# Performance work log

Measured on AMD Instinct MI355X. Metric: run time of the kernel, lower is better.

Reference implementation:

```python
import jax, jax.numpy as jnp
import numpy as np
from jax import lax

SFREQ = 250.0
ORDER = 4
BANDS = [(4.0, 8.0), (8.0, 12.0), (12.0, 16.0), (16.0, 20.0), (20.0, 24.0), (24.0, 28.0), (28.0, 32.0), (32.0, 36.0), (36.0, 40.0)]
KLEN = int(SFREQ // 2)
if KLEN % 2 == 0:
    KLEN += 1  # 125 taps, odd -> same-length output with pad K//2


def _butter_bandpass(order, low, high, sfreq):
    # numpy reimplementation of scipy.signal.butter(order, [low,high]/nyq, btype='band')
    nyq = sfreq / 2.0
    fs = 2.0
    warped = 2.0 * fs * np.tan(np.pi * np.array([low, high]) / nyq / fs)
    m = np.arange(-order + 1, order, 2)
    p = -np.exp(1j * np.pi * m / (2 * order))  # analog Butterworth LP prototype poles
    k = 1.0
    bw = warped[1] - warped[0]
    wo = np.sqrt(warped[0] * warped[1])
    p_lp = p * bw / 2.0
    p_bp = np.concatenate([p_lp + np.sqrt(p_lp ** 2 - wo ** 2), p_lp - np.sqrt(p_lp ** 2 - wo ** 2)])
    z_bp = np.zeros(order, dtype=complex)
    k_bp = k * bw ** order
    fs2 = 2.0 * fs  # bilinear transform
    z_d = (fs2 + z_bp) / (fs2 - z_bp)
    p_d = (fs2 + p_bp) / (fs2 - p_bp)
    z_d = np.append(z_d, -np.ones(len(p_bp) - len(z_bp)))
    k_d = k_bp * np.real(np.prod(fs2 - z_bp) / np.prod(fs2 - p_bp))
    b = np.real(k_d * np.poly(z_d))
    a = np.real(np.poly(p_d))
    return b, a


def _make_kernel(low, high):
    # IIR impulse response (centered impulse, as in the torch module), Hann window, L1 normalize
    b, a = _butter_bandpass(ORDER, low, high, SFREQ)
    x = np.zeros(KLEN)
    x[KLEN // 2] = 1.0
    h = np.zeros(KLEN)
    for n in range(KLEN):
        s = 0.0
        for i in range(len(b)):
            if n - i >= 0:
                s += b[i] * x[n - i]
        for j in range(1, len(a)):
            if n - j >= 0:
                s -= a[j] * h[n - j]
        h[n] = s / a[0]
    nn = np.arange(KLEN)
    h = h * (0.5 - 0.5 * np.cos(2.0 * np.pi * nn / (KLEN - 1)))  # symmetric Hann
    return h / np.sum(np.abs(h))


def setup_inputs() -> dict:
    key = jax.random.key(0)
    x = jax.random.normal(key, (64, 64, 1000), dtype=jnp.float32)  # (B, C, T) EEG
    kernels = jnp.asarray(np.stack([_make_kernel(lo, hi) for lo, hi in BANDS]), dtype=jnp.float32)  # (n_bands, K)
    return {"x": x, "kernels": kernels}


def reference(x, kernels):
    # out[b, i, c, t] = cross-correlation of channel c with band-i kernel (torch Conv1d semantics)
    B, C, T = x.shape
    nb, K = kernels.shape
    pad = K // 2
    x2 = x.reshape(B * C, 1, T)
    w = kernels[:, None, :]  # (n_bands, 1, K)
    y = lax.conv_general_dilated(x2, w, (1,), [(pad, pad)], dimension_numbers=("NCH", "OIH", "NCH"))
    return y.reshape(B, C, nb, T).transpose(0, 2, 1, 3)  # (B, n_bands, C, T)
```

## Files before the change

### kernel.cpp

```cpp
#include <hip/hip_runtime.h>
#include <hip/hip_bf16.h>


#define T_LEN    1000
#define NB       9
#define S_COPY   1160
#define SLOTS    145
#define WT_STRIDE 136

typedef __attribute__((ext_vector_type(8))) short short8;
typedef __attribute__((ext_vector_type(4))) float f32x4;

__device__ __forceinline__ unsigned int f2bf(float f) {
    union { __hip_bfloat16 h; unsigned short u; } cv;
    cv.h = __float2bfloat16(f);
    return (unsigned int)cv.u;
}

__global__ __launch_bounds__(256) void fbank_mfma(
    const float* __restrict__ x,
    const float* __restrict__ kern,
    float* __restrict__ out)
{
    __shared__ unsigned short xs[8 * S_COPY];
    __shared__ unsigned short wt[16 * WT_STRIDE];

    const int tid = threadIdx.x;
    const int bid = blockIdx.x;
    const int bc  = ((bid & 7) << 9) + (bid >> 3);
    const int b   = bc >> 6, c = bc & 63;
    const float* xrow = x + (size_t)bc * T_LEN;

    {
        const int band = tid >> 4, k0 = (tid & 15) << 3;
        unsigned int d[4];
        #pragma unroll
        for (int e2 = 0; e2 < 4; ++e2) {
            int k = k0 + 2 * e2;
            float v0 = (band < NB && k < 125)     ? kern[band * 125 + k]     : 0.f;
            float v1 = (band < NB && k + 1 < 125) ? kern[band * 125 + k + 1] : 0.f;
            d[e2] = f2bf(v0) | (f2bf(v1) << 16);
        }
        *reinterpret_cast<uint4*>(&wt[band * WT_STRIDE + k0]) =
            make_uint4(d[0], d[1], d[2], d[3]);
    }

    {
        const int r = tid >> 5, q0 = tid & 31;
        #pragma unroll
        for (int i = 0; i < 5; ++i) {
            int q = q0 + 32 * i;
            if (q < SLOTS) {
                int idx0 = 8 * q + r - 64;
                unsigned int d[4];
                #pragma unroll
                for (int e2 = 0; e2 < 4; ++e2) {
                    int i0 = idx0 + 2 * e2, i1 = i0 + 1;
                    float v0 = ((unsigned)i0 < T_LEN) ? xrow[i0] : 0.f;
                    float v1 = ((unsigned)i1 < T_LEN) ? xrow[i1] : 0.f;
                    d[e2] = f2bf(v0) | (f2bf(v1) << 16);
                }
                *reinterpret_cast<uint4*>(&xs[r * S_COPY + 8 * q]) =
                    make_uint4(d[0], d[1], d[2], d[3]);
            }
        }
    }

    const int lane = tid & 63;
    const int wid  = tid >> 6;
    const int n = lane & 15, g = lane >> 4;

    __syncthreads();

    short8 bt[4];
    #pragma unroll
    for (int kk = 0; kk < 4; ++kk)
        bt[kk] = *reinterpret_cast<const short8*>(wt + n * WT_STRIDE + kk * 32 + g * 8);

    const int t0w = wid << 8;
    const int rl  = (n + 2) & 7;
    const char* xsb = reinterpret_cast<const char*>(xs);
    const int LB = 2 * (1159 * rl + 2 + n + 8 * g + t0w);

    short8 F[8];
    #pragma unroll
    for (int u = 0; u < 6; ++u)
        F[u] = *reinterpret_cast<const short8*>(xsb + LB + 32 * u);

    f32x4 acc[16];
    #pragma unroll
    for (int m = 0; m < 16; ++m) {
        F[(m + 6) & 7] = *reinterpret_cast<const short8*>(xsb + LB + 32 * (m + 6));
        f32x4 a = {0.f, 0.f, 0.f, 0.f};
        #pragma unroll
        for (int kk = 0; kk < 4; ++kk)
            a = __builtin_amdgcn_mfma_f32_16x16x32_bf16(F[(m + 2 * kk) & 7], bt[kk], a, 0, 0, 0);
        acc[m] = a;
    }

    const bool bandok = (n < NB);
    float* obase = out + ((size_t)(b * NB + n) * 64 + c) * T_LEN + t0w + 4 * g;
    #pragma unroll
    for (int m = 0; m < 16; ++m) {
        const int t4 = t0w + 16 * m + 4 * g;
        if (bandok && t4 + 4 <= T_LEN)
            *reinterpret_cast<f32x4*>(obase + 16 * m) = acc[m];
    }
}

extern "C" void kernel_launch(void* const* d_in, const int* in_sizes, int n_in,
                              void* d_out, int out_size, void* d_ws, size_t ws_size,
                              hipStream_t stream) {
    const float* x    = (const float*)d_in[0];
    const float* kern = (const float*)d_in[1];
    float* out = (float*)d_out;

    fbank_mfma<<<64 * 64, 256, 0, stream>>>(x, kern, out);
}
```

Baseline: 56.86 us.

## Load input windows directly from global memory instead of LDS staging

Removes the shared-memory staging of the bf16-converted input row (8 shifted copies) and has each lane load its 8-sample window straight from global memory, converting to bf16 in registers before each MFMA. This drops the LDS writes and most of the pre-barrier staging work. In exchange each lane issues many overlapping, unaligned global loads and repeats the bf16 conversion, relying on L1/L2 caching for reuse across lanes and waves.

```diff
diff --git a/kernel.cpp b/kernel.cpp
--- a/kernel.cpp
+++ b/kernel.cpp
@@ -2,14 +2,13 @@
 #include <hip/hip_bf16.h>
 
 
-#define T_LEN    1000
-#define NB       9
-#define S_COPY   1160
-#define SLOTS    145
+#define T_LEN     1000
+#define NB        9
 #define WT_STRIDE 136
 
 typedef __attribute__((ext_vector_type(8))) short short8;
 typedef __attribute__((ext_vector_type(4))) float f32x4;
+typedef float f32x4a __attribute__((ext_vector_type(4), aligned(4)));
 
 __device__ __forceinline__ unsigned int f2bf(float f) {
     union { __hip_bfloat16 h; unsigned short u; } cv;
@@ -17,12 +16,34 @@
     return (unsigned int)cv.u;
 }
 
+__device__ __forceinline__ short8 load_win(const float* __restrict__ xrow,
+                                           int xi0, bool safe) {
+    float v[8];
+    if (safe) {
+        f32x4a a = *reinterpret_cast<const f32x4a*>(xrow + xi0);
+        f32x4a b = *reinterpret_cast<const f32x4a*>(xrow + xi0 + 4);
+        v[0] = a.x; v[1] = a.y; v[2] = a.z; v[3] = a.w;
+        v[4] = b.x; v[5] = b.y; v[6] = b.z; v[7] = b.w;
+    } else {
+        #pragma unroll
+        for (int e = 0; e < 8; ++e) {
+            int xi = xi0 + e;
+            v[e] = ((unsigned)xi < T_LEN) ? xrow[xi] : 0.f;
+        }
+    }
+    union { uint4 u4; short8 s8; } cv;
+    cv.u4 = make_uint4(f2bf(v[0]) | (f2bf(v[1]) << 16),
+                       f2bf(v[2]) | (f2bf(v[3]) << 16),
+                       f2bf(v[4]) | (f2bf(v[5]) << 16),
+                       f2bf(v[6]) | (f2bf(v[7]) << 16));
+    return cv.s8;
+}
+
 __global__ __launch_bounds__(256) void fbank_mfma(
     const float* __restrict__ x,
     const float* __restrict__ kern,
     float* __restrict__ out)
 {
-    __shared__ unsigned short xs[8 * S_COPY];
     __shared__ unsigned short wt[16 * WT_STRIDE];
 
     const int tid = threadIdx.x;
@@ -45,27 +66,6 @@
             make_uint4(d[0], d[1], d[2], d[3]);
     }
 
-    {
-        const int r = tid >> 5, q0 = tid & 31;
-        #pragma unroll
-        for (int i = 0; i < 5; ++i) {
-            int q = q0 + 32 * i;
-            if (q < SLOTS) {
-                int idx0 = 8 * q + r - 64;
-                unsigned int d[4];
-                #pragma unroll
-                for (int e2 = 0; e2 < 4; ++e2) {
-                    int i0 = idx0 + 2 * e2, i1 = i0 + 1;
-                    float v0 = ((unsigned)i0 < T_LEN) ? xrow[i0] : 0.f;
-                    float v1 = ((unsigned)i1 < T_LEN) ? xrow[i1] : 0.f;
-                    d[e2] = f2bf(v0) | (f2bf(v1) << 16);
-                }
-                *reinterpret_cast<uint4*>(&xs[r * S_COPY + 8 * q]) =
-                    make_uint4(d[0], d[1], d[2], d[3]);
-            }
-        }
-    }
-
     const int lane = tid & 63;
     const int wid  = tid >> 6;
     const int n = lane & 15, g = lane >> 4;
@@ -78,19 +78,21 @@
         bt[kk] = *reinterpret_cast<const short8*>(wt + n * WT_STRIDE + kk * 32 + g * 8);
 
     const int t0w = wid << 8;
-    const int rl  = (n + 2) & 7;
-    const char* xsb = reinterpret_cast<const char*>(xs);
-    const int LB = 2 * (1159 * rl + 2 + n + 8 * g + t0w);
+    const int xi_base = t0w + 2 + n + 8 * g - 64;
 
     short8 F[8];
     #pragma unroll
-    for (int u = 0; u < 6; ++u)
-        F[u] = *reinterpret_cast<const short8*>(xsb + LB + 32 * u);
+    for (int u = 0; u < 6; ++u) {
+        const bool safe = (t0w + 16 * u >= 62) && (t0w + 16 * u <= 1015);
+        F[u] = load_win(xrow, xi_base + 16 * u, safe);
+    }
 
     f32x4 acc[16];
     #pragma unroll
     for (int m = 0; m < 16; ++m) {
-        F[(m + 6) & 7] = *reinterpret_cast<const short8*>(xsb + LB + 32 * (m + 6));
+        const int u = m + 6;
+        const bool safe = (t0w + 16 * u >= 62) && (t0w + 16 * u <= 1015);
+        F[u & 7] = load_win(xrow, xi_base + 16 * u, safe);
         f32x4 a = {0.f, 0.f, 0.f, 0.f};
         #pragma unroll
         for (int kk = 0; kk < 4; ++kk)
```

After: 65.19 us. +14.6%, slower.
